# Optimization experiments

Hardware: AMD Instinct MI355X
Metric: run time of the kernel (lower is better)

The kernel has to match this reference:

```python
import jax, jax.numpy as jnp
from jax import lax
import numpy as np

B, HI, WI = 8, 56, 56
HO, WO = HI // 2, WI // 2
DIN, DOUT = 96, 192
N_IN, N_OUT = HI * WI, HO * WO
HD = 32
NH = DOUT // HD
H2, W2, N2 = HO, WO, HO * WO
NA_W = 7
NUM_ITERS, DEPTH = 3, 2


def _build_group_tables():
    # M_loc: 0 inside 3x3 output window around each input token, -1e4 elsewhere
    # qidx: which of the 9 relative offsets maps (input i -> output j); -1 outside window
    mask = np.full((N_IN, N_OUT), -1e4, np.float32)
    idx = np.full((N_IN, N_OUT), -1, np.int64)
    rr, cc = np.meshgrid(np.arange(HI), np.arange(WI), indexing='ij')
    rr, cc = rr.ravel(), cc.ravel()
    r0, c0 = rr // 2, cc // 2
    ii = np.arange(N_IN)
    offs = [(dr, dc) for dr in (-1, 0, 1) for dc in (-1, 0, 1)]
    for kk, (dr, dc) in enumerate(offs):
        oi = np.clip(r0 + dr, 0, HO - 1) * WO + np.clip(c0 + dc, 0, WO - 1)
        mask[ii, oi] = 0.0
        idx[ii, oi] = kk
    # torch rpb[-1] == rpb[8]; emulate negative indexing with %9
    return jnp.asarray(mask), jnp.asarray(idx % 9)

M_LOC, QIDX = _build_group_tables()


def _rope_tables(n, d):
    inv = 1.0 / (10000.0 ** (np.arange(0, d, 2, dtype=np.float32) / d))
    ang = np.outer(np.arange(n, dtype=np.float32), inv)
    return jnp.asarray(np.cos(ang), jnp.float32), jnp.asarray(np.sin(ang), jnp.float32)

ROPE_COS, ROPE_SIN = _rope_tables(N2, HD)


def _na_idx(n, w):
    # NATTEN-style shifted windows: center clamped so the window stays in-bounds
    half = w // 2
    c = np.clip(np.arange(n), half, n - 1 - half)
    return jnp.asarray(c[:, None] + np.arange(-half, half + 1)[None, :])

NB_R = _na_idx(H2, NA_W)
NB_C = _na_idx(W2, NA_W)


def _ln(x, g, b):
    m = x.mean(-1, keepdims=True)
    v = ((x - m) ** 2).mean(-1, keepdims=True)
    return (x - m) / jnp.sqrt(v + 1e-5) * g + b


def _rope(t):  # t: [B, N, heads, head_dim]
    b, n, h, d = t.shape
    tr = t.reshape(b, n, h, d // 2, 2)
    x0, x1 = tr[..., 0], tr[..., 1]
    c = ROPE_COS[None, :, None, :]
    s = ROPE_SIN[None, :, None, :]
    return jnp.stack([x0 * c - x1 * s, x1 * c + x0 * s], -1).reshape(b, n, h, d)


def _forward(x, seed_conv_w, q_proj_w, k_proj_w, v_proj_w, g_ln_in_g, g_ln_in_b, g_ln_out_g, g_ln_out_b, g_ln_attn_g, g_ln_attn_b, g_ln_mlp_g, g_ln_mlp_b, g_mlp_w1, g_mlp_b1, g_mlp_w2, g_mlp_b2, tau, rpb, blk_ln1_g, blk_ln1_b, blk_ln2_g, blk_ln2_b, blk_qkv_w, blk_proj_w, blk_proj_b, blk_mlp_w1, blk_mlp_b1, blk_mlp_w2, blk_mlp_b2):
    b = x.shape[0]
    # ---- SparseGroupingLayer (local/sparse path), eval mode ----
    xc = x.transpose(0, 2, 1).reshape(b, DIN, HI, WI)
    seed = lax.conv_general_dilated(xc, seed_conv_w, (2, 2), ((1, 1), (1, 1)), dimension_numbers=('NCHW', 'OIHW', 'NCHW'))
    x_out = _ln(seed.reshape(b, DOUT, N_OUT).transpose(0, 2, 1), g_ln_out_g, g_ln_out_b)
    xn = _ln(x, g_ln_in_g, g_ln_in_b)
    k = xn @ k_proj_w.T
    v = xn @ v_proj_w.T
    bias = rpb[QIDX] + M_LOC  # [N_in, N_out]
    scale = jnp.exp(tau[0])
    for _ in range(NUM_ITERS):
        q = _ln(x_out, g_ln_out_g, g_ln_out_b) @ q_proj_w.T  # [B, N_out, dim_in]
        logits = jnp.einsum('bnd,bmd->bnm', k, q) * scale + bias[None]
        a_ups = jax.nn.softmax(logits, -1)
        a_down = a_ups / (a_ups.sum(1, keepdims=True) + 1e-8)
        upd = jnp.einsum('bnm,bnd->bmd', a_down, v)
        x_out = x_out + _ln(upd, g_ln_attn_g, g_ln_attn_b)
        h = jax.nn.gelu(x_out @ g_mlp_w1.T + g_mlp_b1, approximate=False) @ g_mlp_w2.T + g_mlp_b2
        x_out = x_out + _ln(h, g_ln_mlp_g, g_ln_mlp_b)
    # ---- SeNaTraBlocks: neighborhood attention (window=7) + RoPE, eval mode ----
    rows = NB_R[:, None, :, None]
    cols = NB_C[None, :, None, :]
    for i in range(DEPTH):
        xb = _ln(x_out, blk_ln1_g[i], blk_ln1_b[i])
        qkv = (xb @ blk_qkv_w[i].T).reshape(b, N2, 3, NH, HD)
        q = _rope(qkv[:, :, 0]).transpose(0, 2, 1, 3).reshape(b, NH, H2, W2, HD)
        kk = _rope(qkv[:, :, 1]).transpose(0, 2, 1, 3).reshape(b, NH, H2, W2, HD)
        vv = qkv[:, :, 2].transpose(0, 2, 1, 3).reshape(b, NH, H2, W2, HD)
        kn = kk[:, :, rows, cols].reshape(b, NH, H2, W2, NA_W * NA_W, HD)
        vn = vv[:, :, rows, cols].reshape(b, NH, H2, W2, NA_W * NA_W, HD)
        att = jnp.einsum('bhijd,bhijkd->bhijk', q, kn) * (HD ** -0.5)
        att = jax.nn.softmax(att, -1)
        o = jnp.einsum('bhijk,bhijkd->bhijd', att, vn)
        o = o.reshape(b, NH, N2, HD).transpose(0, 2, 1, 3).reshape(b, N2, DOUT)
        x_out = x_out + (o @ blk_proj_w[i].T + blk_proj_b[i])
        xb = _ln(x_out, blk_ln2_g[i], blk_ln2_b[i])
        h = jax.nn.gelu(xb @ blk_mlp_w1[i].T + blk_mlp_b1[i], approximate=False) @ blk_mlp_w2[i].T + blk_mlp_b2[i]
        x_out = x_out + h
    return x_out


def setup_inputs() -> dict:
    key = jax.random.key(0)
    ks = jax.random.split(key, 12)
    hid_g, hid_b = 2 * DOUT, 3 * DOUT
    def rn(k, shape, s=0.02):
        return jax.random.normal(k, shape, jnp.float32) * s
    return {
        'x': jax.random.normal(ks[0], (B, N_IN, DIN), jnp.float32),
        'seed_conv_w': rn(ks[1], (DOUT, DIN, 3, 3), 0.05),
        'q_proj_w': rn(ks[2], (DIN, DOUT)),
        'k_proj_w': rn(ks[3], (DIN, DIN)),
        'v_proj_w': rn(ks[4], (DOUT, DIN)),
        'g_ln_in_g': jnp.ones((DIN,), jnp.float32), 'g_ln_in_b': jnp.zeros((DIN,), jnp.float32),
        'g_ln_out_g': jnp.ones((DOUT,), jnp.float32), 'g_ln_out_b': jnp.zeros((DOUT,), jnp.float32),
        'g_ln_attn_g': jnp.ones((DOUT,), jnp.float32), 'g_ln_attn_b': jnp.zeros((DOUT,), jnp.float32),
        'g_ln_mlp_g': jnp.ones((DOUT,), jnp.float32), 'g_ln_mlp_b': jnp.zeros((DOUT,), jnp.float32),
        'g_mlp_w1': rn(ks[5], (hid_g, DOUT)), 'g_mlp_b1': jnp.zeros((hid_g,), jnp.float32),
        'g_mlp_w2': rn(ks[6], (DOUT, hid_g)), 'g_mlp_b2': jnp.zeros((DOUT,), jnp.float32),
        'tau': jnp.array([float(np.log(DIN ** -0.5))], jnp.float32),
        'rpb': rn(ks[7], (9,)),
        'blk_ln1_g': jnp.ones((DEPTH, DOUT), jnp.float32), 'blk_ln1_b': jnp.zeros((DEPTH, DOUT), jnp.float32),
        'blk_ln2_g': jnp.ones((DEPTH, DOUT), jnp.float32), 'blk_ln2_b': jnp.zeros((DEPTH, DOUT), jnp.float32),
        'blk_qkv_w': rn(ks[8], (DEPTH, 3 * DOUT, DOUT)),
        'blk_proj_w': rn(ks[9], (DEPTH, DOUT, DOUT)), 'blk_proj_b': jnp.zeros((DEPTH, DOUT), jnp.float32),
        'blk_mlp_w1': rn(ks[10], (DEPTH, hid_b, DOUT)), 'blk_mlp_b1': jnp.zeros((DEPTH, hid_b), jnp.float32),
        'blk_mlp_w2': rn(ks[11], (DEPTH, DOUT, hid_b)), 'blk_mlp_b2': jnp.zeros((DEPTH, DOUT), jnp.float32),
    }


def reference(x, seed_conv_w, q_proj_w, k_proj_w, v_proj_w, g_ln_in_g, g_ln_in_b, g_ln_out_g, g_ln_out_b, g_ln_attn_g, g_ln_attn_b, g_ln_mlp_g, g_ln_mlp_b, g_mlp_w1, g_mlp_b1, g_mlp_w2, g_mlp_b2, tau, rpb, blk_ln1_g, blk_ln1_b, blk_ln2_g, blk_ln2_b, blk_qkv_w, blk_proj_w, blk_proj_b, blk_mlp_w1, blk_mlp_b1, blk_mlp_w2, blk_mlp_b2):
    return _forward(x, seed_conv_w, q_proj_w, k_proj_w, v_proj_w, g_ln_in_g, g_ln_in_b, g_ln_out_g, g_ln_out_b, g_ln_attn_g, g_ln_attn_b, g_ln_mlp_g, g_ln_mlp_b, g_mlp_w1, g_mlp_b1, g_mlp_w2, g_mlp_b2, tau, rpb, blk_ln1_g, blk_ln1_b, blk_ln2_g, blk_ln2_b, blk_qkv_w, blk_proj_w, blk_proj_b, blk_mlp_w1, blk_mlp_b1, blk_mlp_w2, blk_mlp_b2)
```

## Files before the change

kernel.cpp:

```cpp
#include <hip/hip_runtime.h>
#include <hip/hip_bf16.h>

#define DEV __device__ __forceinline__

typedef __attribute__((ext_vector_type(8))) short short8;
typedef __attribute__((ext_vector_type(4))) float f32x4;

DEV unsigned short f2b(float f) {
  union { float f; unsigned u; } v; v.f = f;
  unsigned r = v.u + 0x7FFFu + ((v.u >> 16) & 1u);
  return (unsigned short)(r >> 16);
}
DEV float b2f16(unsigned short b) {
  union { unsigned u; float f; } v; v.u = ((unsigned)b) << 16;
  return v.f;
}

__global__ void k_castw(const float* __restrict__ s0, const float* __restrict__ s1,
    const float* __restrict__ s2, const float* __restrict__ s3,
    const float* __restrict__ s4, const float* __restrict__ s5,
    const float* __restrict__ s6, const float* __restrict__ s7,
    const float* __restrict__ s8, const float* __restrict__ s9,
    short* __restrict__ dh, short* __restrict__ dl) {
  int idx = blockIdx.x * 256 + threadIdx.x;
  if (idx >= 1096704) return;
  float v;
  if (idx < 165888) {
    int co = idx / 864, rem = idx % 864;
    int k9 = rem / 96, ci = rem % 96;
    v = s0[co * 864 + ci * 9 + k9];
  } else {
    const float* src; int base;
    if      (idx < 175104) { src = s1; base = 165888; }
    else if (idx < 193536) { src = s2; base = 175104; }
    else if (idx < 211968) { src = s3; base = 193536; }
    else if (idx < 285696) { src = s4; base = 211968; }
    else if (idx < 359424) { src = s5; base = 285696; }
    else if (idx < 580608) { src = s6; base = 359424; }
    else if (idx < 654336) { src = s7; base = 580608; }
    else if (idx < 875520) { src = s8; base = 654336; }
    else                   { src = s9; base = 875520; }
    v = src[idx - base];
  }
  unsigned short h = f2b(v);
  dh[idx] = (short)h;
  dl[idx] = (short)f2b(v - b2f16(h));
}

__global__ void k_rope(float* ct, float* st) {
  int idx = blockIdx.x * 256 + threadIdx.x;
  if (idx >= 784 * 16) return;
  int n = idx >> 4, j = idx & 15;
  float inv = powf(10000.f, -(float)(2 * j) / 32.f);
  float ang = (float)n * inv;
  ct[idx] = cosf(ang);
  st[idx] = sinf(ang);
}

template<int D>
__global__ __launch_bounds__(256) void k_ln(const float* __restrict__ in,
    const float* __restrict__ g, const float* __restrict__ b,
    float* __restrict__ out, int M) {
  int tok = blockIdx.x * 4 + (threadIdx.x >> 6);
  int l = threadIdx.x & 63;
  if (tok >= M) return;
  const float* row = in + (size_t)tok * D;
  constexpr int E = (D + 63) / 64;
  float v[E];
  float s = 0.f, s2 = 0.f;
#pragma unroll
  for (int e = 0; e < E; ++e) {
    int i = e * 64 + l;
    float x = (i < D) ? row[i] : 0.f;
    v[e] = x; s += x; s2 += x * x;
  }
  for (int off = 32; off; off >>= 1) { s += __shfl_xor(s, off); s2 += __shfl_xor(s2, off); }
  float mean = s / D, var = s2 / D - mean * mean;
  float rstd = rsqrtf(var + 1e-5f);
  float* orow = out + (size_t)tok * D;
#pragma unroll
  for (int e = 0; e < E; ++e) {
    int i = e * 64 + l;
    if (i < D) orow[i] = (v[e] - mean) * rstd * g[i] + b[i];
  }
}

template<int ADD>
__global__ __launch_bounds__(256) void k_ln_epi(const float* __restrict__ raw,
    const float* __restrict__ g, const float* __restrict__ b,
    float* __restrict__ out, int M) {
  int tok = blockIdx.x * 4 + (threadIdx.x >> 6);
  int l = threadIdx.x & 63;
  if (tok >= M) return;
  const float* row = raw + (size_t)tok * 192;
  float v[3];
  float s = 0.f, s2 = 0.f;
#pragma unroll
  for (int e = 0; e < 3; ++e) {
    float x = row[e * 64 + l];
    v[e] = x; s += x; s2 += x * x;
  }
  for (int off = 32; off; off >>= 1) { s += __shfl_xor(s, off); s2 += __shfl_xor(s2, off); }
  float mean = s / 192.f, var = s2 / 192.f - mean * mean;
  float rstd = rsqrtf(var + 1e-5f);
  float* orow = out + (size_t)tok * 192;
#pragma unroll
  for (int e = 0; e < 3; ++e) {
    int i = e * 64 + l;
    float r = (v[e] - mean) * rstd * g[i] + b[i];
    if (ADD) orow[i] += r; else orow[i] = r;
  }
}

template<int EPI, int CONV>
__global__ __launch_bounds__(256) void k_mgemm(
    const float* __restrict__ A, const short* __restrict__ WH,
    const short* __restrict__ WL, const float* __restrict__ bias,
    float* __restrict__ C, int M, int N, int K,
    const float* __restrict__ ct, const float* __restrict__ st,
    float* __restrict__ o1, float* __restrict__ o2, float* __restrict__ o3) {
  __shared__ short AsH[64][40], AsL[64][40];
  __shared__ short BsH[64][40], BsL[64][40];
  int t = threadIdx.x;
  int m0 = blockIdx.x * 64, n0 = blockIdx.y * 64;
  int sr = t >> 2, sq = (t & 3) * 8;
  int lane = t & 63, w = t >> 6, wm = w >> 1, wn = w & 1;
  int fr = lane & 15, fq = lane >> 4;
  f32x4 acc[2][2];
#pragma unroll
  for (int i = 0; i < 2; ++i)
#pragma unroll
    for (int j = 0; j < 2; ++j) acc[i][j] = (f32x4){0.f, 0.f, 0.f, 0.f};

  for (int kt = 0; kt < K; kt += 32) {
    short8 vh, vl;
    if (CONV) {
      int m = m0 + sr;
      int b = m / 784, rm = m % 784, ho = rm / 28, wo = rm % 28;
      int k = kt + sq;
      int k9 = k / 96, ci0 = k % 96;
      int hi = 2 * ho - 1 + k9 / 3, wi = 2 * wo - 1 + k9 % 3;
      if (hi >= 0 && hi < 56 && wi >= 0 && wi < 56) {
        const float* src = &A[((size_t)b * 3136 + hi * 56 + wi) * 96 + ci0];
        float4 a0 = *(const float4*)src;
        float4 a1 = *(const float4*)(src + 4);
        float av[8] = {a0.x, a0.y, a0.z, a0.w, a1.x, a1.y, a1.z, a1.w};
#pragma unroll
        for (int j = 0; j < 8; ++j) {
          unsigned short h = f2b(av[j]);
          vh[j] = (short)h;
          vl[j] = (short)f2b(av[j] - b2f16(h));
        }
      } else {
#pragma unroll
        for (int j = 0; j < 8; ++j) { vh[j] = 0; vl[j] = 0; }
      }
    } else {
      const float4 a0 = *(const float4*)&A[(size_t)(m0 + sr) * K + kt + sq];
      const float4 a1 = *(const float4*)&A[(size_t)(m0 + sr) * K + kt + sq + 4];
      float av[8] = {a0.x, a0.y, a0.z, a0.w, a1.x, a1.y, a1.z, a1.w};
#pragma unroll
      for (int j = 0; j < 8; ++j) {
        unsigned short h = f2b(av[j]);
        vh[j] = (short)h;
        vl[j] = (short)f2b(av[j] - b2f16(h));
      }
    }
    *(short8*)&AsH[sr][sq] = vh;
    *(short8*)&AsL[sr][sq] = vl;
    {
      int n = n0 + sr;
      if (n < N) {
        *(short8*)&BsH[sr][sq] = *(const short8*)&WH[(size_t)n * K + kt + sq];
        *(short8*)&BsL[sr][sq] = *(const short8*)&WL[(size_t)n * K + kt + sq];
      } else {
        short8 z = {0, 0, 0, 0, 0, 0, 0, 0};
        *(short8*)&BsH[sr][sq] = z;
        *(short8*)&BsL[sr][sq] = z;
      }
    }
    __syncthreads();
    short8 ah[2], al[2], bh[2], bl[2];
#pragma unroll
    for (int s = 0; s < 2; ++s) {
      ah[s] = *(const short8*)&AsH[wm * 32 + s * 16 + fr][fq * 8];
      al[s] = *(const short8*)&AsL[wm * 32 + s * 16 + fr][fq * 8];
      bh[s] = *(const short8*)&BsH[wn * 32 + s * 16 + fr][fq * 8];
      bl[s] = *(const short8*)&BsL[wn * 32 + s * 16 + fr][fq * 8];
    }
#pragma unroll
    for (int i = 0; i < 2; ++i)
#pragma unroll
      for (int j = 0; j < 2; ++j) {
        acc[i][j] = __builtin_amdgcn_mfma_f32_16x16x32_bf16(ah[i], bh[j], acc[i][j], 0, 0, 0);
        acc[i][j] = __builtin_amdgcn_mfma_f32_16x16x32_bf16(ah[i], bl[j], acc[i][j], 0, 0, 0);
        acc[i][j] = __builtin_amdgcn_mfma_f32_16x16x32_bf16(al[i], bh[j], acc[i][j], 0, 0, 0);
      }
    __syncthreads();
  }
#pragma unroll
  for (int i = 0; i < 2; ++i) {
#pragma unroll
    for (int j = 0; j < 2; ++j) {
      int n = n0 + wn * 32 + j * 16 + fr;
#pragma unroll
      for (int r = 0; r < 4; ++r) {
        int m = m0 + wm * 32 + i * 16 + fq * 4 + r;
        float v = acc[i][j][r];
        float pa = 0.f;
        if (EPI == 3) pa = __shfl_xor(v, 1);
        if (n >= N) continue;
        if (bias) v += bias[n];
        if (EPI == 1) v = 0.5f * v * (1.f + erff(v * 0.70710678118654752f));
        if (EPI == 3) {
          int sec = n / 192, d = n % 192, h = d / 32, dh = d % 32;
          int b = m / 784, mm = m % 784;
          float val;
          if (sec < 2) {
            int jj = dh >> 1;
            float cc = ct[mm * 16 + jj], ss = st[mm * 16 + jj];
            val = (dh & 1) ? (v * cc + pa * ss) : (v * cc - pa * ss);
          } else val = v;
          float* dst = (sec == 0) ? o1 : ((sec == 1) ? o2 : o3);
          dst[(((size_t)b * 6 + h) * 784 + mm) * 32 + dh] = val;
        } else if (EPI == 2) {
          C[(size_t)m * N + n] += v;
        } else {
          C[(size_t)m * N + n] = v;
        }
      }
      if (EPI == 4 && n < N) {
        int mb = m0 + wm * 32 + i * 16 + fq * 4;
        float4 tv = make_float4(acc[i][j][0], acc[i][j][1], acc[i][j][2], acc[i][j][3]);
        *(float4*)&o1[(size_t)n * M + mb] = tv;
      }
    }
  }
}

__global__ void k_pass1(const float* __restrict__ kkT, const float* __restrict__ q,
    const float* __restrict__ rpb, const float* __restrict__ tau,
    float* __restrict__ M, float* __restrict__ Z) {
  int id = blockIdx.x * 256 + threadIdx.x;
  if (id >= 8 * 3136) return;
  int b = id / 3136, n = id % 3136;
  int r = n / 56, c = n % 56, r0 = r >> 1, c0 = c >> 1;
  int oi[9];
#pragma unroll
  for (int kki = 0; kki < 9; ++kki) {
    int dr = kki / 3 - 1, dc = kki % 3 - 1;
    int rr = min(max(r0 + dr, 0), 27), cc = min(max(c0 + dc, 0), 27);
    oi[kki] = rr * 28 + cc;
  }
  float scale = expf(tau[0]);
  float lg[9]; bool keep[9];
  float mx = -1e30f;
#pragma unroll
  for (int kki = 0; kki < 9; ++kki) {
    bool kp = true;
#pragma unroll
    for (int k2 = kki + 1; k2 < 9; ++k2) if (oi[k2] == oi[kki]) kp = false;
    keep[kki] = kp;
    if (kp) {
      const float* qr = q + ((size_t)b * 784 + oi[kki]) * 96;
      float d = 0.f;
      for (int i = 0; i < 96; ++i) d += kkT[(size_t)i * 25088 + id] * qr[i];
      lg[kki] = d * scale + rpb[kki];
      mx = fmaxf(mx, lg[kki]);
    } else lg[kki] = -1e30f;
  }
  float z = 0.f;
#pragma unroll
  for (int kki = 0; kki < 9; ++kki) if (keep[kki]) z += expf(lg[kki] - mx);
  M[id] = mx; Z[id] = z;
}

__global__ __launch_bounds__(192) void k_pass2(const float* __restrict__ kk,
    const float* __restrict__ q, const float* __restrict__ vv,
    const float* __restrict__ M, const float* __restrict__ Z,
    const float* __restrict__ rpb, const float* __restrict__ tau,
    const float* __restrict__ g, const float* __restrict__ bb, float* __restrict__ xout) {
  int blk = blockIdx.x, b = blk / 784, m = blk % 784;
  int r2 = m / 28, c2 = m % 28;
  int r0lo = (r2 == 0) ? 0 : r2 - 1, r0hi = (r2 == 27) ? 27 : r2 + 1;
  int c0lo = (c2 == 0) ? 0 : c2 - 1, c0hi = (c2 == 27) ? 27 : c2 + 1;
  int nrow = 2 * (r0hi - r0lo + 1), ncol = 2 * (c0hi - c0lo + 1);
  int cnt = nrow * ncol;
  __shared__ float qm[96], p[36];
  __shared__ int nlist[36];
  __shared__ float2 red[192];
  int t = threadIdx.x;
  if (t < 96) qm[t] = q[(size_t)blk * 96 + t];
  __syncthreads();
  if (t < cnt) {
    int rr = 2 * r0lo + t / ncol, cc = 2 * c0lo + t % ncol;
    int n = rr * 56 + cc, rr0 = rr >> 1, cc0 = cc >> 1;
    int kkf = 0;
#pragma unroll
    for (int kki = 0; kki < 9; ++kki) {
      int dr = kki / 3 - 1, dc = kki % 3 - 1;
      int ra = min(max(rr0 + dr, 0), 27), ca = min(max(cc0 + dc, 0), 27);
      if (ra == r2 && ca == c2) kkf = kki;
    }
    const float* krow = kk + ((size_t)b * 3136 + n) * 96;
    float d = 0.f;
    for (int i = 0; i < 96; ++i) d += krow[i] * qm[i];
    float scale = expf(tau[0]);
    float lg = d * scale + rpb[kkf];
    size_t idn = (size_t)b * 3136 + n;
    p[t] = expf(lg - M[idn]) / Z[idn];
    nlist[t] = n;
  }
  __syncthreads();
  float denom = 0.f;
  for (int jn = 0; jn < cnt; ++jn) denom += p[jn];
  float acc = 0.f;
  for (int jn = 0; jn < cnt; ++jn)
    acc += p[jn] * vv[((size_t)b * 3136 + nlist[jn]) * 192 + t];
  float upd = acc / (denom + 1e-8f);
  red[t] = make_float2(upd, upd * upd);
  __syncthreads();
  for (int s = 128; s > 0; s >>= 1) {
    if (t < s && t + s < 192) { red[t].x += red[t + s].x; red[t].y += red[t + s].y; }
    __syncthreads();
  }
  float mean = red[0].x / 192.f, var = red[0].y / 192.f - mean * mean;
  float rstd = rsqrtf(var + 1e-5f);
  xout[(size_t)blk * 192 + t] += (upd - mean) * rstd * g[t] + bb[t];
}

__global__ __launch_bounds__(256) void k_attn(const float* __restrict__ q3,
    const float* __restrict__ k3, const float* __restrict__ v3, float* __restrict__ ob) {
  int bid = blockIdx.x;
  int swz = (bid & 7) * 1176 + (bid >> 3);
  int unit = swz * 4 + (threadIdx.x >> 6);
  int l = threadIdx.x & 63;
  int b = unit / (6 * 784), rem = unit % (6 * 784), h = rem / 784, m = rem % 784;
  int i = m / 28, j = m % 28;
  int ib = min(max(i, 3), 24) - 3, jb = min(max(j, 3), 24) - 3;
  size_t base = (size_t)(b * 6 + h) * 784 * 32;
  const float4* q4 = (const float4*)(q3 + base + (size_t)m * 32);
  float4 qv[8];
#pragma unroll
  for (int e = 0; e < 8; ++e) qv[e] = q4[e];
  float logit = -1e30f;
  if (l < 49) {
    int nk = (ib + l / 7) * 28 + (jb + l % 7);
    const float4* k4 = (const float4*)(k3 + base + (size_t)nk * 32);
    float a = 0.f;
#pragma unroll
    for (int e = 0; e < 8; ++e) {
      float4 kv = k4[e];
      a += qv[e].x * kv.x + qv[e].y * kv.y + qv[e].z * kv.z + qv[e].w * kv.w;
    }
    logit = a * 0.17677669529663687f;
  }
  float mx = logit;
  for (int off = 32; off; off >>= 1) mx = fmaxf(mx, __shfl_xor(mx, off));
  float p = (l < 49) ? expf(logit - mx) : 0.f;
  float sum = p;
  for (int off = 32; off; off >>= 1) sum += __shfl_xor(sum, off);
  int half = l >> 5, d = l & 31;
  int kbeg = half ? 25 : 0, kend = half ? 49 : 25;
  float acc = 0.f;
  for (int kki = kbeg; kki < kend; ++kki) {
    float pk = __shfl(p, kki);
    int nk = (ib + kki / 7) * 28 + (jb + kki % 7);
    acc += pk * v3[base + (size_t)nk * 32 + d];
  }
  acc += __shfl_xor(acc, 32);
  if (l < 32)
    ob[(((size_t)b * 784 + m) * 6 + h) * 32 + l] = acc / sum;
}

extern "C" void kernel_launch(void* const* d_in, const int* in_sizes, int n_in,
                              void* d_out, int out_size, void* d_ws, size_t ws_size,
                              hipStream_t stream) {
  (void)in_sizes; (void)n_in; (void)out_size; (void)ws_size;
  const float* x        = (const float*)d_in[0];
  const float* convw    = (const float*)d_in[1];
  const float* qw       = (const float*)d_in[2];
  const float* kw       = (const float*)d_in[3];
  const float* vw       = (const float*)d_in[4];
  const float* ln_in_g  = (const float*)d_in[5];
  const float* ln_in_b  = (const float*)d_in[6];
  const float* ln_out_g = (const float*)d_in[7];
  const float* ln_out_b = (const float*)d_in[8];
  const float* ln_at_g  = (const float*)d_in[9];
  const float* ln_at_b  = (const float*)d_in[10];
  const float* ln_ml_g  = (const float*)d_in[11];
  const float* ln_ml_b  = (const float*)d_in[12];
  const float* gw1      = (const float*)d_in[13];
  const float* gb1      = (const float*)d_in[14];
  const float* gw2      = (const float*)d_in[15];
  const float* gb2      = (const float*)d_in[16];
  const float* tau      = (const float*)d_in[17];
  const float* rpb      = (const float*)d_in[18];
  const float* bln1g    = (const float*)d_in[19];
  const float* bln1b    = (const float*)d_in[20];
  const float* bln2g    = (const float*)d_in[21];
  const float* bln2b    = (const float*)d_in[22];
  const float* bqkvw    = (const float*)d_in[23];
  const float* bprojw   = (const float*)d_in[24];
  const float* bprojb   = (const float*)d_in[25];
  const float* bmw1     = (const float*)d_in[26];
  const float* bmb1     = (const float*)d_in[27];
  const float* bmw2     = (const float*)d_in[28];
  const float* bmb2     = (const float*)d_in[29];

  float* XOUT = (float*)d_out;

  float* W = (float*)d_ws;
  size_t off = 0;
  float* XN96  = W + off; off += (size_t)25088 * 96;
  float* XN192 = W + off; off += (size_t)6272 * 192;
  float* Kb    = W + off; off += (size_t)25088 * 96;
  float* KbT   = W + off; off += (size_t)25088 * 96;
  float* Vb    = W + off; off += (size_t)25088 * 192;
  float* Qb    = W + off; off += (size_t)6272 * 96;
  float* Mb    = W + off; off += (size_t)25088;
  float* Zb    = W + off; off += (size_t)25088;
  float* H1    = W + off; off += (size_t)6272 * 576;
  float* T2    = W + off; off += (size_t)6272 * 192;
  float* CT    = W + off; off += (size_t)784 * 16;
  float* ST    = W + off; off += (size_t)784 * 16;
  short* WBH   = (short*)(W + off); off += (size_t)548352 + 16;
  short* WBL   = (short*)(W + off); off += (size_t)548352 + 16;
  const size_t O_c = 0, O_k = 165888, O_v = 175104, O_q = 193536,
               O_g1 = 211968, O_g2 = 285696, O_qkv = 359424, O_p = 580608,
               O_m1 = 654336, O_m2 = 875520;
  float* CRAW = T2;
  float* Q3 = Kb;
  float* K3 = KbT;
  float* V3 = Vb;
  float* OB = Vb + (size_t)1204224;

  k_castw<<<4284, 256, 0, stream>>>(convw, kw, vw, qw, gw1, gw2, bqkvw, bprojw,
                                    bmw1, bmw2, WBH, WBL);
  k_rope<<<49, 256, 0, stream>>>(CT, ST);

  k_mgemm<0, 1><<<dim3(98, 3), 256, 0, stream>>>(x, WBH + O_c, WBL + O_c, nullptr,
      CRAW, 6272, 192, 864, nullptr, nullptr, nullptr, nullptr, nullptr);
  k_ln_epi<0><<<1568, 256, 0, stream>>>(CRAW, ln_out_g, ln_out_b, XOUT, 6272);

  k_ln<96><<<6272, 256, 0, stream>>>(x, ln_in_g, ln_in_b, XN96, 25088);
  k_mgemm<4, 0><<<dim3(392, 2), 256, 0, stream>>>(XN96, WBH + O_k, WBL + O_k, nullptr,
      Kb, 25088, 96, 96, nullptr, nullptr, KbT, nullptr, nullptr);
  k_mgemm<0, 0><<<dim3(392, 3), 256, 0, stream>>>(XN96, WBH + O_v, WBL + O_v, nullptr,
      Vb, 25088, 192, 96, nullptr, nullptr, nullptr, nullptr, nullptr);

  for (int it = 0; it < 3; ++it) {
    k_ln<192><<<1568, 256, 0, stream>>>(XOUT, ln_out_g, ln_out_b, XN192, 6272);
    k_mgemm<0, 0><<<dim3(98, 2), 256, 0, stream>>>(XN192, WBH + O_q, WBL + O_q, nullptr,
        Qb, 6272, 96, 192, nullptr, nullptr, nullptr, nullptr, nullptr);
    k_pass1<<<98, 256, 0, stream>>>(KbT, Qb, rpb, tau, Mb, Zb);
    k_pass2<<<6272, 192, 0, stream>>>(Kb, Qb, Vb, Mb, Zb, rpb, tau, ln_at_g, ln_at_b, XOUT);
    k_mgemm<1, 0><<<dim3(98, 6), 256, 0, stream>>>(XOUT, WBH + O_g1, WBL + O_g1, gb1,
        H1, 6272, 384, 192, nullptr, nullptr, nullptr, nullptr, nullptr);
    k_mgemm<0, 0><<<dim3(98, 3), 256, 0, stream>>>(H1, WBH + O_g2, WBL + O_g2, gb2,
        T2, 6272, 192, 384, nullptr, nullptr, nullptr, nullptr, nullptr);
    k_ln_epi<1><<<1568, 256, 0, stream>>>(T2, ln_ml_g, ln_ml_b, XOUT, 6272);
  }

  for (int i = 0; i < 2; ++i) {
    k_ln<192><<<1568, 256, 0, stream>>>(XOUT, bln1g + (size_t)i * 192,
                                        bln1b + (size_t)i * 192, XN192, 6272);
    k_mgemm<3, 0><<<dim3(98, 9), 256, 0, stream>>>(XN192, WBH + O_qkv + (size_t)i * 110592,
        WBL + O_qkv + (size_t)i * 110592, nullptr,
        nullptr, 6272, 576, 192, CT, ST, Q3, K3, V3);
    k_attn<<<9408, 256, 0, stream>>>(Q3, K3, V3, OB);
    k_mgemm<2, 0><<<dim3(98, 3), 256, 0, stream>>>(OB, WBH + O_p + (size_t)i * 36864,
        WBL + O_p + (size_t)i * 36864, bprojb + (size_t)i * 192,
        XOUT, 6272, 192, 192, nullptr, nullptr, nullptr, nullptr, nullptr);
    k_ln<192><<<1568, 256, 0, stream>>>(XOUT, bln2g + (size_t)i * 192,
                                        bln2b + (size_t)i * 192, XN192, 6272);
    k_mgemm<1, 0><<<dim3(98, 9), 256, 0, stream>>>(XN192, WBH + O_m1 + (size_t)i * 110592,
        WBL + O_m1 + (size_t)i * 110592, bmb1 + (size_t)i * 576,
        H1, 6272, 576, 192, nullptr, nullptr, nullptr, nullptr, nullptr);
    k_mgemm<2, 0><<<dim3(98, 3), 256, 0, stream>>>(H1, WBH + O_m2 + (size_t)i * 110592,
        WBL + O_m2 + (size_t)i * 110592, bmb2 + (size_t)i * 192,
        XOUT, 6272, 192, 576, nullptr, nullptr, nullptr, nullptr, nullptr);
  }
}
```

Baseline: 745.8 us.

## Fuse layernorm apply into GEMM A-loads and process two queries per attention wave

```diff
diff --git a/kernel.cpp b/kernel.cpp
--- a/kernel.cpp
+++ b/kernel.cpp
@@ -58,31 +58,23 @@
 }
 
 template<int D>
-__global__ __launch_bounds__(256) void k_ln(const float* __restrict__ in,
-    const float* __restrict__ g, const float* __restrict__ b,
-    float* __restrict__ out, int M) {
+__global__ __launch_bounds__(256) void k_lnstat(const float* __restrict__ in,
+    float2* __restrict__ stats, int M) {
   int tok = blockIdx.x * 4 + (threadIdx.x >> 6);
   int l = threadIdx.x & 63;
   if (tok >= M) return;
   const float* row = in + (size_t)tok * D;
   constexpr int E = (D + 63) / 64;
-  float v[E];
   float s = 0.f, s2 = 0.f;
 #pragma unroll
   for (int e = 0; e < E; ++e) {
     int i = e * 64 + l;
     float x = (i < D) ? row[i] : 0.f;
-    v[e] = x; s += x; s2 += x * x;
+    s += x; s2 += x * x;
   }
   for (int off = 32; off; off >>= 1) { s += __shfl_xor(s, off); s2 += __shfl_xor(s2, off); }
   float mean = s / D, var = s2 / D - mean * mean;
-  float rstd = rsqrtf(var + 1e-5f);
-  float* orow = out + (size_t)tok * D;
-#pragma unroll
-  for (int e = 0; e < E; ++e) {
-    int i = e * 64 + l;
-    if (i < D) orow[i] = (v[e] - mean) * rstd * g[i] + b[i];
-  }
+  if (l == 0) stats[tok] = make_float2(mean, rsqrtf(var + 1e-5f));
 }
 
 template<int ADD>
@@ -112,11 +104,13 @@
   }
 }
 
-template<int EPI, int CONV>
+template<int EPI, int CONV, int LNS>
 __global__ __launch_bounds__(256) void k_mgemm(
     const float* __restrict__ A, const short* __restrict__ WH,
     const short* __restrict__ WL, const float* __restrict__ bias,
     float* __restrict__ C, int M, int N, int K,
+    const float2* __restrict__ lnstats, const float* __restrict__ lng,
+    const float* __restrict__ lnb,
     const float* __restrict__ ct, const float* __restrict__ st,
     float* __restrict__ o1, float* __restrict__ o2, float* __restrict__ o3) {
   __shared__ short AsH[64][40], AsL[64][40];
@@ -126,6 +120,8 @@
   int sr = t >> 2, sq = (t & 3) * 8;
   int lane = t & 63, w = t >> 6, wm = w >> 1, wn = w & 1;
   int fr = lane & 15, fq = lane >> 4;
+  float2 lst = make_float2(0.f, 1.f);
+  if (LNS) lst = lnstats[m0 + sr];
   f32x4 acc[2][2];
 #pragma unroll
   for (int i = 0; i < 2; ++i)
@@ -161,6 +157,7 @@
       float av[8] = {a0.x, a0.y, a0.z, a0.w, a1.x, a1.y, a1.z, a1.w};
 #pragma unroll
       for (int j = 0; j < 8; ++j) {
+        if (LNS) av[j] = (av[j] - lst.x) * lst.y * lng[kt + sq + j] + lnb[kt + sq + j];
         unsigned short h = f2b(av[j]);
         vh[j] = (short)h;
         vl[j] = (short)f2b(av[j] - b2f16(h));
@@ -332,45 +329,67 @@
 __global__ __launch_bounds__(256) void k_attn(const float* __restrict__ q3,
     const float* __restrict__ k3, const float* __restrict__ v3, float* __restrict__ ob) {
   int bid = blockIdx.x;
-  int swz = (bid & 7) * 1176 + (bid >> 3);
+  int swz = (bid & 7) * 588 + (bid >> 3);
   int unit = swz * 4 + (threadIdx.x >> 6);
   int l = threadIdx.x & 63;
-  int b = unit / (6 * 784), rem = unit % (6 * 784), h = rem / 784, m = rem % 784;
-  int i = m / 28, j = m % 28;
-  int ib = min(max(i, 3), 24) - 3, jb = min(max(j, 3), 24) - 3;
-  size_t base = (size_t)(b * 6 + h) * 784 * 32;
-  const float4* q4 = (const float4*)(q3 + base + (size_t)m * 32);
-  float4 qv[8];
-#pragma unroll
-  for (int e = 0; e < 8; ++e) qv[e] = q4[e];
-  float logit = -1e30f;
+  int p0 = unit * 2;
+  int bh = p0 / 784;
+  int m0 = p0 % 784, m1 = m0 + 1;
+  size_t base = (size_t)bh * 784 * 32;
+  const float4* q40 = (const float4*)(q3 + base + (size_t)m0 * 32);
+  const float4* q41 = (const float4*)(q3 + base + (size_t)m1 * 32);
+  float4 qa[8], qb[8];
+#pragma unroll
+  for (int e = 0; e < 8; ++e) { qa[e] = q40[e]; qb[e] = q41[e]; }
+  int i0 = m0 / 28, j0 = m0 % 28, i1 = m1 / 28, j1 = m1 % 28;
+  int ib0 = min(max(i0, 3), 24) - 3, jb0 = min(max(j0, 3), 24) - 3;
+  int ib1 = min(max(i1, 3), 24) - 3, jb1 = min(max(j1, 3), 24) - 3;
+  float lg0 = -1e30f, lg1 = -1e30f;
   if (l < 49) {
-    int nk = (ib + l / 7) * 28 + (jb + l % 7);
-    const float4* k4 = (const float4*)(k3 + base + (size_t)nk * 32);
-    float a = 0.f;
+    int dr = l / 7, dc = l % 7;
+    const float4* k40 = (const float4*)(k3 + base + (size_t)((ib0 + dr) * 28 + jb0 + dc) * 32);
+    const float4* k41 = (const float4*)(k3 + base + (size_t)((ib1 + dr) * 28 + jb1 + dc) * 32);
+    float a0 = 0.f, a1 = 0.f;
 #pragma unroll
     for (int e = 0; e < 8; ++e) {
-      float4 kv = k4[e];
-      a += qv[e].x * kv.x + qv[e].y * kv.y + qv[e].z * kv.z + qv[e].w * kv.w;
+      float4 kv0 = k40[e], kv1 = k41[e];
+      a0 += qa[e].x * kv0.x + qa[e].y * kv0.y + qa[e].z * kv0.z + qa[e].w * kv0.w;
+      a1 += qb[e].x * kv1.x + qb[e].y * kv1.y + qb[e].z * kv1.z + qb[e].w * kv1.w;
     }
-    logit = a * 0.17677669529663687f;
-  }
-  float mx = logit;
-  for (int off = 32; off; off >>= 1) mx = fmaxf(mx, __shfl_xor(mx, off));
-  float p = (l < 49) ? expf(logit - mx) : 0.f;
-  float sum = p;
-  for (int off = 32; off; off >>= 1) sum += __shfl_xor(sum, off);
+    lg0 = a0 * 0.17677669529663687f;
+    lg1 = a1 * 0.17677669529663687f;
+  }
+  float mx0 = lg0, mx1 = lg1;
+  for (int off = 32; off; off >>= 1) {
+    mx0 = fmaxf(mx0, __shfl_xor(mx0, off));
+    mx1 = fmaxf(mx1, __shfl_xor(mx1, off));
+  }
+  float p0v = (l < 49) ? expf(lg0 - mx0) : 0.f;
+  float p1v = (l < 49) ? expf(lg1 - mx1) : 0.f;
+  float s0 = p0v, s1 = p1v;
+  for (int off = 32; off; off >>= 1) {
+    s0 += __shfl_xor(s0, off);
+    s1 += __shfl_xor(s1, off);
+  }
   int half = l >> 5, d = l & 31;
   int kbeg = half ? 25 : 0, kend = half ? 49 : 25;
-  float acc = 0.f;
+  float ac0 = 0.f, ac1 = 0.f;
   for (int kki = kbeg; kki < kend; ++kki) {
-    float pk = __shfl(p, kki);
-    int nk = (ib + kki / 7) * 28 + (jb + kki % 7);
-    acc += pk * v3[base + (size_t)nk * 32 + d];
-  }
-  acc += __shfl_xor(acc, 32);
-  if (l < 32)
-    ob[(((size_t)b * 784 + m) * 6 + h) * 32 + l] = acc / sum;
+    float pk0 = __shfl(p0v, kki);
+    float pk1 = __shfl(p1v, kki);
+    int dr = kki / 7, dc = kki % 7;
+    int nk0 = (ib0 + dr) * 28 + jb0 + dc;
+    int nk1 = (ib1 + dr) * 28 + jb1 + dc;
+    ac0 += pk0 * v3[base + (size_t)nk0 * 32 + d];
+    ac1 += pk1 * v3[base + (size_t)nk1 * 32 + d];
+  }
+  ac0 += __shfl_xor(ac0, 32);
+  ac1 += __shfl_xor(ac1, 32);
+  if (l < 32) {
+    int b = bh / 6, h = bh % 6;
+    ob[(((size_t)b * 784 + m0) * 6 + h) * 32 + l] = ac0 / s0;
+    ob[(((size_t)b * 784 + m1) * 6 + h) * 32 + l] = ac1 / s1;
+  }
 }
 
 extern "C" void kernel_launch(void* const* d_in, const int* in_sizes, int n_in,
@@ -412,8 +431,6 @@
 
   float* W = (float*)d_ws;
   size_t off = 0;
-  float* XN96  = W + off; off += (size_t)25088 * 96;
-  float* XN192 = W + off; off += (size_t)6272 * 192;
   float* Kb    = W + off; off += (size_t)25088 * 96;
   float* KbT   = W + off; off += (size_t)25088 * 96;
   float* Vb    = W + off; off += (size_t)25088 * 192;
@@ -424,6 +441,8 @@
   float* T2    = W + off; off += (size_t)6272 * 192;
   float* CT    = W + off; off += (size_t)784 * 16;
   float* ST    = W + off; off += (size_t)784 * 16;
+  float2* S96  = (float2*)(W + off); off += (size_t)25088 * 2;
+  float2* S192 = (float2*)(W + off); off += (size_t)6272 * 2;
   short* WBH   = (short*)(W + off); off += (size_t)548352 + 16;
   short* WBL   = (short*)(W + off); off += (size_t)548352 + 16;
   const size_t O_c = 0, O_k = 165888, O_v = 175104, O_q = 193536,
@@ -439,46 +458,54 @@
                                     bmw1, bmw2, WBH, WBL);
   k_rope<<<49, 256, 0, stream>>>(CT, ST);
 
-  k_mgemm<0, 1><<<dim3(98, 3), 256, 0, stream>>>(x, WBH + O_c, WBL + O_c, nullptr,
-      CRAW, 6272, 192, 864, nullptr, nullptr, nullptr, nullptr, nullptr);
+  k_mgemm<0, 1, 0><<<dim3(98, 3), 256, 0, stream>>>(x, WBH + O_c, WBL + O_c, nullptr,
+      CRAW, 6272, 192, 864, nullptr, nullptr, nullptr,
+      nullptr, nullptr, nullptr, nullptr, nullptr);
   k_ln_epi<0><<<1568, 256, 0, stream>>>(CRAW, ln_out_g, ln_out_b, XOUT, 6272);
 
-  k_ln<96><<<6272, 256, 0, stream>>>(x, ln_in_g, ln_in_b, XN96, 25088);
-  k_mgemm<4, 0><<<dim3(392, 2), 256, 0, stream>>>(XN96, WBH + O_k, WBL + O_k, nullptr,
-      Kb, 25088, 96, 96, nullptr, nullptr, KbT, nullptr, nullptr);
-  k_mgemm<0, 0><<<dim3(392, 3), 256, 0, stream>>>(XN96, WBH + O_v, WBL + O_v, nullptr,
-      Vb, 25088, 192, 96, nullptr, nullptr, nullptr, nullptr, nullptr);
+  k_lnstat<96><<<6272, 256, 0, stream>>>(x, S96, 25088);
+  k_mgemm<4, 0, 1><<<dim3(392, 2), 256, 0, stream>>>(x, WBH + O_k, WBL + O_k, nullptr,
+      Kb, 25088, 96, 96, S96, ln_in_g, ln_in_b,
+      nullptr, nullptr, KbT, nullptr, nullptr);
+  k_mgemm<0, 0, 1><<<dim3(392, 3), 256, 0, stream>>>(x, WBH + O_v, WBL + O_v, nullptr,
+      Vb, 25088, 192, 96, S96, ln_in_g, ln_in_b,
+      nullptr, nullptr, nullptr, nullptr, nullptr);
 
   for (int it = 0; it < 3; ++it) {
-    k_ln<192><<<1568, 256, 0, stream>>>(XOUT, ln_out_g, ln_out_b, XN192, 6272);
-    k_mgemm<0, 0><<<dim3(98, 2), 256, 0, stream>>>(XN192, WBH + O_q, WBL + O_q, nullptr,
-        Qb, 6272, 96, 192, nullptr, nullptr, nullptr, nullptr, nullptr);
+    k_lnstat<192><<<1568, 256, 0, stream>>>(XOUT, S192, 6272);
+    k_mgemm<0, 0, 1><<<dim3(98, 2), 256, 0, stream>>>(XOUT, WBH + O_q, WBL + O_q, nullptr,
+        Qb, 6272, 96, 192, S192, ln_out_g, ln_out_b,
+        nullptr, nullptr, nullptr, nullptr, nullptr);
     k_pass1<<<98, 256, 0, stream>>>(KbT, Qb, rpb, tau, Mb, Zb);
     k_pass2<<<6272, 192, 0, stream>>>(Kb, Qb, Vb, Mb, Zb, rpb, tau, ln_at_g, ln_at_b, XOUT);
-    k_mgemm<1, 0><<<dim3(98, 6), 256, 0, stream>>>(XOUT, WBH + O_g1, WBL + O_g1, gb1,
-        H1, 6272, 384, 192, nullptr, nullptr, nullptr, nullptr, nullptr);
-    k_mgemm<0, 0><<<dim3(98, 3), 256, 0, stream>>>(H1, WBH + O_g2, WBL + O_g2, gb2,
-        T2, 6272, 192, 384, nullptr, nullptr, nullptr, nullptr, nullptr);
+    k_mgemm<1, 0, 0><<<dim3(98, 6), 256, 0, stream>>>(XOUT, WBH + O_g1, WBL + O_g1, gb1,
+        H1, 6272, 384, 192, nullptr, nullptr, nullptr,
+        nullptr, nullptr, nullptr, nullptr, nullptr);
+    k_mgemm<0, 0, 0><<<dim3(98, 3), 256, 0, stream>>>(H1, WBH + O_g2, WBL + O_g2, gb2,
+        T2, 6272, 192, 384, nullptr, nullptr, nullptr,
+        nullptr, nullptr, nullptr, nullptr, nullptr);
     k_ln_epi<1><<<1568, 256, 0, stream>>>(T2, ln_ml_g, ln_ml_b, XOUT, 6272);
   }
 
   for (int i = 0; i < 2; ++i) {
-    k_ln<192><<<1568, 256, 0, stream>>>(XOUT, bln1g + (size_t)i * 192,
-                                        bln1b + (size_t)i * 192, XN192, 6272);
-    k_mgemm<3, 0><<<dim3(98, 9), 256, 0, stream>>>(XN192, WBH + O_qkv + (size_t)i * 110592,
+    k_lnstat<192><<<1568, 256, 0, stream>>>(XOUT, S192, 6272);
+    k_mgemm<3, 0, 1><<<dim3(98, 9), 256, 0, stream>>>(XOUT, WBH + O_qkv + (size_t)i * 110592,
         WBL + O_qkv + (size_t)i * 110592, nullptr,
-        nullptr, 6272, 576, 192, CT, ST, Q3, K3, V3);
-    k_attn<<<9408, 256, 0, stream>>>(Q3, K3, V3, OB);
-    k_mgemm<2, 0><<<dim3(98, 3), 256, 0, stream>>>(OB, WBH + O_p + (size_t)i * 36864,
+        nullptr, 6272, 576, 192, S192, bln1g + (size_t)i * 192, bln1b + (size_t)i * 192,
+        CT, ST, Q3, K3, V3);
+    k_attn<<<4704, 256, 0, stream>>>(Q3, K3, V3, OB);
+    k_mgemm<2, 0, 0><<<dim3(98, 3), 256, 0, stream>>>(OB, WBH + O_p + (size_t)i * 36864,
         WBL + O_p + (size_t)i * 36864, bprojb + (size_t)i * 192,
-        XOUT, 6272, 192, 192, nullptr, nullptr, nullptr, nullptr, nullptr);
-    k_ln<192><<<1568, 256, 0, stream>>>(XOUT, bln2g + (size_t)i * 192,
-                                        bln2b + (size_t)i * 192, XN192, 6272);
-    k_mgemm<1, 0><<<dim3(98, 9), 256, 0, stream>>>(XN192, WBH + O_m1 + (size_t)i * 110592,
+        XOUT, 6272, 192, 192, nullptr, nullptr, nullptr,
+        nullptr, nullptr, nullptr, nullptr, nullptr);
+    k_lnstat<192><<<1568, 256, 0, stream>>>(XOUT, S192, 6272);
+    k_mgemm<1, 0, 1><<<dim3(98, 9), 256, 0, stream>>>(XOUT, WBH + O_m1 + (size_t)i * 110592,
         WBL + O_m1 + (size_t)i * 110592, bmb1 + (size_t)i * 576,
-        H1, 6272, 576, 192, nullptr, nullptr, nullptr, nullptr, nullptr);
-    k_mgemm<2, 0><<<dim3(98, 3), 256, 0, stream>>>(H1, WBH + O_m2 + (size_t)i * 110592,
+        H1, 6272, 576, 192, S192, bln2g + (size_t)i * 192, bln2b + (size_t)i * 192,
+        nullptr, nullptr, nullptr, nullptr, nullptr);
+    k_mgemm<2, 0, 0><<<dim3(98, 3), 256, 0, stream>>>(H1, WBH + O_m2 + (size_t)i * 110592,
         WBL + O_m2 + (size_t)i * 110592, bmb2 + (size_t)i * 192,
-        XOUT, 6272, 192, 576, nullptr, nullptr, nullptr, nullptr, nullptr);
-  }
-}
+        XOUT, 6272, 192, 576, nullptr, nullptr, nullptr,
+        nullptr, nullptr, nullptr, nullptr, nullptr);
+  }
+}
```

After: 748.3 us. No clear change (+0.3%).
